# Kernel tuning notes

Measured on AMD Instinct MI355X. Metric: run time of the kernel, lower is better.

## Reference

```python
import jax, jax.numpy as jnp
import numpy as np

RANK = 16
ALPHA = 32
SCALING = ALPHA / RANK  # alpha / rank


def setup_inputs() -> dict:
    key = jax.random.key(0)
    k_x, k_w, k_b, k_a, k_bb = jax.random.split(key, 5)
    B, S, D_IN, D_OUT = 4, 2048, 4096, 4096
    x = jax.random.normal(k_x, (B, S, D_IN), dtype=jnp.float32)
    W = jax.random.normal(k_w, (D_OUT, D_IN), dtype=jnp.float32) * (1.0 / np.sqrt(D_IN))
    b = jax.random.normal(k_b, (D_OUT,), dtype=jnp.float32) * 0.02
    # LoRA init: A ~ N(0, 2/rank); B is zeros in the module, but we use small
    # random values so the adapter path is numerically exercised.
    lora_A = jax.random.normal(k_a, (RANK, D_IN), dtype=jnp.float32) * np.sqrt(2.0 / RANK)
    lora_B = jax.random.normal(k_bb, (D_OUT, RANK), dtype=jnp.float32) * 0.02
    return {"x": x, "W": W, "b": b, "lora_A": lora_A, "lora_B": lora_B}


def reference(x, W, b, lora_A, lora_B):
    # Base linear: x @ W^T + b
    base = jnp.einsum("bsd,od->bso", x, W) + b
    # LoRA path, fused as two rank-r matmuls (never materializing B@A):
    # (x @ A^T) @ B^T * scaling  ==  F.linear(x, B@A) * scaling
    xa = jnp.einsum("bsd,rd->bsr", x, lora_A)      # [B,S,r]
    lora = jnp.einsum("bsr,or->bso", xa, lora_B)    # [B,S,D_out]
    return base + lora * SCALING
```

## Files before the change

kernel.cpp:

```cpp
#include <hip/hip_runtime.h>
#include <hip/hip_bf16.h>

#define K_DIM 4096
#define N_DIM 4096
#define R_DIM 16
#define SCALING_F 2.0f

#define BM 256
#define BN 256
#define BK 64

typedef __attribute__((ext_vector_type(8))) short bf16x8;
typedef __attribute__((ext_vector_type(16))) float f32x16;

__device__ __forceinline__ ushort f2bf(float f) {
  union { float f; unsigned u; } v; v.f = f;
  unsigned u = v.u;
  u += 0x7FFF + ((u >> 16) & 1);
  return (ushort)(u >> 16);
}

__global__ __launch_bounds__(256) void prepass_kernel(
    const float* __restrict__ x, ushort* __restrict__ xb,
    const float* __restrict__ W, const float* __restrict__ A,
    const float* __restrict__ Bl, ushort* __restrict__ wb, long n4) {
  if (blockIdx.x < N_DIM) {
    int o = blockIdx.x;
    float breg[R_DIM];
#pragma unroll
    for (int r = 0; r < R_DIM; ++r) breg[r] = Bl[o * R_DIM + r] * SCALING_F;
    for (int d0 = threadIdx.x * 4; d0 < K_DIM; d0 += blockDim.x * 4) {
      float4 w = *(const float4*)(W + (size_t)o * K_DIM + d0);
      float a0 = w.x, a1 = w.y, a2 = w.z, a3 = w.w;
#pragma unroll
      for (int r = 0; r < R_DIM; ++r) {
        float4 a = *(const float4*)(A + (size_t)r * K_DIM + d0);
        a0 += breg[r] * a.x; a1 += breg[r] * a.y;
        a2 += breg[r] * a.z; a3 += breg[r] * a.w;
      }
      ushort4 ob;
      ob.x = f2bf(a0); ob.y = f2bf(a1); ob.z = f2bf(a2); ob.w = f2bf(a3);
      *(ushort4*)(wb + (size_t)o * K_DIM + d0) = ob;
    }
  } else {
    long i = (long)(blockIdx.x - N_DIM) * blockDim.x + threadIdx.x;
    long stride = 2048L * blockDim.x;
    for (; i < n4; i += stride) {
      long idx = i * 4;
      float4 v = *(const float4*)(x + idx);
      ushort4 o;
      o.x = f2bf(v.x); o.y = f2bf(v.y); o.z = f2bf(v.z); o.w = f2bf(v.w);
      *(ushort4*)(xb + idx) = o;
    }
  }
}


#define RS 8192L

#define GLOAD(SRC, LOFF)                                                    \
  __builtin_amdgcn_global_load_lds(                                         \
      (const __attribute__((address_space(1))) void*)(SRC),                 \
      (__attribute__((address_space(3))) void*)(smem + (LOFF)), 16, 0, 0)

#define LDSA(BUF) ((BUF) * 32768)
#define LDSB(BUF) (65536 + (BUF) * 32768)

#define ST_A_EVEN(T, BUF) do {                                              \
    GLOAD(aS + (size_t)(T) * 128,            LDSA(BUF) + ldsDst);           \
    GLOAD(aS + (size_t)(T) * 128 + 128 * RS, LDSA(BUF) + 16384 + ldsDst); } while (0)
#define ST_A_ODD(T, BUF) do {                                               \
    GLOAD(aS + (size_t)(T) * 128 + 64 * RS,  LDSA(BUF) + 8192 + ldsDst);    \
    GLOAD(aS + (size_t)(T) * 128 + 192 * RS, LDSA(BUF) + 24576 + ldsDst); } while (0)
#define ST_B_H0(T, BUF) do {                                                \
    GLOAD(bS + (size_t)(T) * 128,            LDSB(BUF) + ldsDst);           \
    GLOAD(bS + (size_t)(T) * 128 + 64 * RS,  LDSB(BUF) + 8192 + ldsDst); } while (0)
#define ST_B_H1(T, BUF) do {                                                \
    GLOAD(bS + (size_t)(T) * 128 + 128 * RS, LDSB(BUF) + 16384 + ldsDst);   \
    GLOAD(bS + (size_t)(T) * 128 + 192 * RS, LDSB(BUF) + 24576 + ldsDst); } while (0)

#define LDAx(MI, KS, BUF) (*(const bf16x8*)(smem + LDSA(BUF) + aRd + (MI) * 4096 + cs##KS))
#define LDBx(NI, KS, BUF) (*(const bf16x8*)(smem + LDSB(BUF) + bRd + (NI) * 4096 + cs##KS))

#define RDB_ALL(BUF) do {                                                   \
    bfr[0][0] = LDBx(0, 0, BUF); bfr[0][1] = LDBx(0, 1, BUF);               \
    bfr[0][2] = LDBx(0, 2, BUF); bfr[0][3] = LDBx(0, 3, BUF);               \
    bfr[1][0] = LDBx(1, 0, BUF); bfr[1][1] = LDBx(1, 1, BUF);               \
    bfr[1][2] = LDBx(1, 2, BUF); bfr[1][3] = LDBx(1, 3, BUF); } while (0)

#define RDA(MB, K0, K1, BUF) do {                                           \
    afr[0][0] = LDAx(MB, K0, BUF);       afr[0][1] = LDAx(MB, K1, BUF);     \
    afr[1][0] = LDAx((MB) + 1, K0, BUF); afr[1][1] = LDAx((MB) + 1, K1, BUF); } while (0)

#define MFMA8(MB, KH) do {                                                  \
    _Pragma("unroll") for (int mm = 0; mm < 2; ++mm)                        \
      _Pragma("unroll") for (int nn = 0; nn < 2; ++nn)                      \
        _Pragma("unroll") for (int kk = 0; kk < 2; ++kk)                    \
          acc[(MB) + mm][nn] = __builtin_amdgcn_mfma_f32_32x32x16_bf16(     \
              afr[mm][kk], bfr[nn][2 * (KH) + kk], acc[(MB) + mm][nn], 0, 0, 0); } while (0)

#define PH_MFMA(MB, KH) do {                                                \
    __builtin_amdgcn_s_barrier();                                           \
    asm volatile("s_waitcnt lgkmcnt(0)" ::: "memory");                      \
    __builtin_amdgcn_s_setprio(1);                                          \
    MFMA8(MB, KH);                                                          \
    __builtin_amdgcn_s_setprio(0); } while (0)

__global__ __launch_bounds__(512, 2) void gemm_lora_kernel(
    const ushort* __restrict__ Ab, const ushort* __restrict__ Bb,
    const float* __restrict__ bias, float* __restrict__ C) {
  __shared__ char smem[131072];

  const int tid = threadIdx.x;
  const int wave = tid >> 6, lane = tid & 63;
  const int wm = wave >> 2, wn = wave & 3;
  const int r31 = lane & 31, hi = lane >> 5;

  const int bid = blockIdx.x;
  const int bm = ((bid & 7) << 2) + ((bid >> 3) & 3);
  const int bn = bid >> 5;

  const int trow = tid >> 3;
  const int tswz = ((tid & 7) << 4) ^ ((trow & 7) << 4);
  const char* aS = (const char*)Ab + (size_t)(bm * BM + trow) * RS + tswz;
  const char* bS = (const char*)Bb + (size_t)(bn * BN + trow) * RS + tswz;
  const int ldsDst = tid << 4;

  const int hi16 = hi << 4;
  const int swz  = (lane & 7) << 4;
  const int cs0 = (0  + hi16) ^ swz;
  const int cs1 = (32 + hi16) ^ swz;
  const int cs2 = (64 + hi16) ^ swz;
  const int cs3 = (96 + hi16) ^ swz;
  const int aRd = (wm * 128 + r31) * 128;
  const int bRd = (wn * 64 + r31) * 128;

  f32x16 acc[4][2];
#pragma unroll
  for (int m = 0; m < 4; ++m)
#pragma unroll
    for (int n = 0; n < 2; ++n)
#pragma unroll
      for (int v = 0; v < 16; ++v) acc[m][n][v] = 0.f;
  bf16x8 afr[2][2], bfr[2][4];

  ST_B_H0(0, 0); ST_B_H1(0, 0); ST_A_EVEN(0, 0); ST_A_ODD(0, 0);
  ST_B_H0(1, 1); ST_B_H1(1, 1); ST_A_EVEN(1, 1);
  asm volatile("s_waitcnt vmcnt(6)" ::: "memory");
  __builtin_amdgcn_s_barrier();

  const int NIT = K_DIM / (2 * BK);
#pragma unroll 1
  for (int i = 0; i < NIT; ++i) {
    const int t1 = 2 * i + 1, t2 = 2 * i + 2, t3 = 2 * i + 3;
    const bool last = (i == NIT - 1);

    RDB_ALL(0);
    RDA(0, 0, 1, 0);
    ST_A_ODD(t1, 1);
    asm volatile("s_waitcnt lgkmcnt(8)" ::: "memory");
    PH_MFMA(0, 0);
    __builtin_amdgcn_s_barrier();

    RDA(0, 2, 3, 0);
    if (!last) ST_B_H0(t2, 0);
    PH_MFMA(0, 1);
    __builtin_amdgcn_s_barrier();

    RDA(2, 0, 1, 0);
    if (!last) ST_B_H1(t2, 0);
    PH_MFMA(2, 0);
    __builtin_amdgcn_s_barrier();

    RDA(2, 2, 3, 0);
    if (!last) ST_A_EVEN(t2, 0);
    PH_MFMA(2, 1);
    if (last) asm volatile("s_waitcnt vmcnt(0)" ::: "memory");
    else      asm volatile("s_waitcnt vmcnt(6)" ::: "memory");
    __builtin_amdgcn_s_barrier();

    RDB_ALL(1);
    RDA(0, 0, 1, 1);
    if (!last) ST_A_ODD(t2, 0);
    asm volatile("s_waitcnt lgkmcnt(8)" ::: "memory");
    PH_MFMA(0, 0);
    __builtin_amdgcn_s_barrier();

    RDA(0, 2, 3, 1);
    if (!last) ST_B_H0(t3, 1);
    PH_MFMA(0, 1);
    __builtin_amdgcn_s_barrier();

    RDA(2, 0, 1, 1);
    if (!last) ST_B_H1(t3, 1);
    PH_MFMA(2, 0);
    __builtin_amdgcn_s_barrier();

    RDA(2, 2, 3, 1);
    if (!last) ST_A_EVEN(t3, 1);
    PH_MFMA(2, 1);
    if (!last) {
      asm volatile("s_waitcnt vmcnt(6)" ::: "memory");
      __builtin_amdgcn_s_barrier();
    }
  }

  const int ccol0 = bn * BN + wn * 64 + r31;
  const float bv0 = bias[ccol0];
  const float bv1 = bias[ccol0 + 32];
  const int crow0 = bm * BM + wm * 128 + hi * 4;
#pragma unroll
  for (int mi = 0; mi < 4; ++mi)
#pragma unroll
    for (int v = 0; v < 16; ++v) {
      int row = crow0 + mi * 32 + (v & 3) + 8 * (v >> 2);
      C[(size_t)row * N_DIM + ccol0]      = acc[mi][0][v] + bv0;
      C[(size_t)row * N_DIM + ccol0 + 32] = acc[mi][1][v] + bv1;
    }
}

extern "C" void kernel_launch(void* const* d_in, const int* in_sizes, int n_in,
                              void* d_out, int out_size, void* d_ws, size_t ws_size,
                              hipStream_t stream) {
  const float* x  = (const float*)d_in[0];
  const float* W  = (const float*)d_in[1];
  const float* b  = (const float*)d_in[2];
  const float* lA = (const float*)d_in[3];
  const float* lB = (const float*)d_in[4];
  float* out = (float*)d_out;

  const int M = in_sizes[0] / K_DIM;

  ushort* xb = (ushort*)d_ws;
  ushort* wb = xb + (size_t)M * K_DIM;

  long n4 = (long)M * K_DIM / 4;
  prepass_kernel<<<N_DIM + 2048, 256, 0, stream>>>(x, xb, W, lA, lB, wb, n4);
  gemm_lora_kernel<<<(M / BM) * (N_DIM / BN), 512, 0, stream>>>(xb, wb, b, out);
}
```

Measured before the change: 340.9 us.

## Prefetch LDS fragments one phase ahead and move swizzle into prepass layout

Moves the XOR swizzle from the LDS load addressing into the global layout written by the bf16 prepass, so each 16-byte global_load_lds copies contiguously. Fragment reads now issue as two 8-byte LDS loads with a new swizzle pattern. A and B register fragments for the next MFMA phase are loaded right after the current phase's MFMAs, which overlaps LDS latency with compute. The vmcnt waits are retuned to match the reordered stores. The risks are more LDS instructions from the split 8-byte reads, possible bank conflicts, and the removed memory clobber on the lgkmcnt wait, which could let the compiler reorder LDS reads past it.

```diff
diff --git a/kernel.cpp b/kernel.cpp
--- a/kernel.cpp
+++ b/kernel.cpp
@@ -10,6 +10,7 @@
 #define BN 256
 #define BK 64
 
+typedef __attribute__((ext_vector_type(4))) short bf16x4;
 typedef __attribute__((ext_vector_type(8))) short bf16x8;
 typedef __attribute__((ext_vector_type(16))) float f32x16;
 
@@ -40,7 +41,8 @@
       }
       ushort4 ob;
       ob.x = f2bf(a0); ob.y = f2bf(a1); ob.z = f2bf(a2); ob.w = f2bf(a3);
-      *(ushort4*)(wb + (size_t)o * K_DIM + d0) = ob;
+      int cs = (d0 >> 2) ^ (o & 15);
+      *(ushort4*)(wb + (size_t)o * K_DIM + (cs << 2)) = ob;
     }
   } else {
     long i = (long)(blockIdx.x - N_DIM) * blockDim.x + threadIdx.x;
@@ -50,7 +52,9 @@
       float4 v = *(const float4*)(x + idx);
       ushort4 o;
       o.x = f2bf(v.x); o.y = f2bf(v.y); o.z = f2bf(v.z); o.w = f2bf(v.w);
-      *(ushort4*)(xb + idx) = o;
+      int row15 = (int)(idx >> 12) & 15;
+      int cs = (((int)idx & 4095) >> 2) ^ row15;
+      *(ushort4*)(xb + (idx & ~4095L) + ((long)cs << 2)) = o;
     }
   }
 }
@@ -79,18 +83,22 @@
     GLOAD(bS + (size_t)(T) * 128 + 128 * RS, LDSB(BUF) + 16384 + ldsDst);   \
     GLOAD(bS + (size_t)(T) * 128 + 192 * RS, LDSB(BUF) + 24576 + ldsDst); } while (0)
 
-#define LDAx(MI, KS, BUF) (*(const bf16x8*)(smem + LDSA(BUF) + aRd + (MI) * 4096 + cs##KS))
-#define LDBx(NI, KS, BUF) (*(const bf16x8*)(smem + LDSB(BUF) + bRd + (NI) * 4096 + cs##KS))
-
-#define RDB_ALL(BUF) do {                                                   \
-    bfr[0][0] = LDBx(0, 0, BUF); bfr[0][1] = LDBx(0, 1, BUF);               \
-    bfr[0][2] = LDBx(0, 2, BUF); bfr[0][3] = LDBx(0, 3, BUF);               \
-    bfr[1][0] = LDBx(1, 0, BUF); bfr[1][1] = LDBx(1, 1, BUF);               \
-    bfr[1][2] = LDBx(1, 2, BUF); bfr[1][3] = LDBx(1, 3, BUF); } while (0)
-
-#define RDA(MB, K0, K1, BUF) do {                                           \
-    afr[0][0] = LDAx(MB, K0, BUF);       afr[0][1] = LDAx(MB, K1, BUF);     \
-    afr[1][0] = LDAx((MB) + 1, K0, BUF); afr[1][1] = LDAx((MB) + 1, K1, BUF); } while (0)
+#define FR(BASE, OFF, KS)                                                   \
+  __builtin_shufflevector(                                                  \
+      *(const bf16x4*)(smem + (BASE) + (OFF) + cl[KS]),                     \
+      *(const bf16x4*)(smem + (BASE) + (OFF) + ch[KS]),                     \
+      0, 1, 2, 3, 4, 5, 6, 7)
+
+#define PF_A(MB, KH, BUF) do {                                              \
+    afr[0][0] = FR(aRow, (MB) * 4096 + (BUF) * 32768, 2 * (KH));            \
+    afr[0][1] = FR(aRow, (MB) * 4096 + (BUF) * 32768, 2 * (KH) + 1);        \
+    afr[1][0] = FR(aRow, ((MB) + 1) * 4096 + (BUF) * 32768, 2 * (KH));      \
+    afr[1][1] = FR(aRow, ((MB) + 1) * 4096 + (BUF) * 32768, 2 * (KH) + 1); } while (0)
+
+#define PF_B_ALL(BUF) do {                                                  \
+    _Pragma("unroll") for (int nt = 0; nt < 2; ++nt)                        \
+      _Pragma("unroll") for (int ks = 0; ks < 4; ++ks)                      \
+        bfr[nt][ks] = FR(bRow, nt * 4096 + (BUF) * 32768, ks); } while (0)
 
 #define MFMA8(MB, KH) do {                                                  \
     _Pragma("unroll") for (int mm = 0; mm < 2; ++mm)                        \
@@ -99,9 +107,9 @@
           acc[(MB) + mm][nn] = __builtin_amdgcn_mfma_f32_32x32x16_bf16(     \
               afr[mm][kk], bfr[nn][2 * (KH) + kk], acc[(MB) + mm][nn], 0, 0, 0); } while (0)
 
-#define PH_MFMA(MB, KH) do {                                                \
+#define PH_CORE(MB, KH) do {                                                \
     __builtin_amdgcn_s_barrier();                                           \
-    asm volatile("s_waitcnt lgkmcnt(0)" ::: "memory");                      \
+    asm volatile("s_waitcnt lgkmcnt(0)");                                   \
     __builtin_amdgcn_s_setprio(1);                                          \
     MFMA8(MB, KH);                                                          \
     __builtin_amdgcn_s_setprio(0); } while (0)
@@ -121,19 +129,22 @@
   const int bn = bid >> 5;
 
   const int trow = tid >> 3;
-  const int tswz = ((tid & 7) << 4) ^ ((trow & 7) << 4);
-  const char* aS = (const char*)Ab + (size_t)(bm * BM + trow) * RS + tswz;
-  const char* bS = (const char*)Bb + (size_t)(bn * BN + trow) * RS + tswz;
+  const char* aS = (const char*)Ab + (size_t)(bm * BM + trow) * RS + ((tid & 7) << 4);
+  const char* bS = (const char*)Bb + (size_t)(bn * BN + trow) * RS + ((tid & 7) << 4);
   const int ldsDst = tid << 4;
 
-  const int hi16 = hi << 4;
-  const int swz  = (lane & 7) << 4;
-  const int cs0 = (0  + hi16) ^ swz;
-  const int cs1 = (32 + hi16) ^ swz;
-  const int cs2 = (64 + hi16) ^ swz;
-  const int cs3 = (96 + hi16) ^ swz;
-  const int aRd = (wm * 128 + r31) * 128;
-  const int bRd = (wn * 64 + r31) * 128;
+  const int sxh = (r31 & 14) << 3;
+  const int sxb = (r31 & 1) << 3;
+  const int cl[4] = {(((0 * 2 + hi) << 4) ^ sxh) | sxb,
+                     (((1 * 2 + hi) << 4) ^ sxh) | sxb,
+                     (((2 * 2 + hi) << 4) ^ sxh) | sxb,
+                     (((3 * 2 + hi) << 4) ^ sxh) | sxb};
+  const int ch[4] = {(((0 * 2 + hi) << 4) ^ sxh) | (8 ^ sxb),
+                     (((1 * 2 + hi) << 4) ^ sxh) | (8 ^ sxb),
+                     (((2 * 2 + hi) << 4) ^ sxh) | (8 ^ sxb),
+                     (((3 * 2 + hi) << 4) ^ sxh) | (8 ^ sxb)};
+  const int aRow = (wm * 128 + r31) * 128;
+  const int bRow = 65536 + (wn * 64 + r31) * 128;
 
   f32x16 acc[4][2];
 #pragma unroll
@@ -148,6 +159,8 @@
   ST_B_H0(1, 1); ST_B_H1(1, 1); ST_A_EVEN(1, 1);
   asm volatile("s_waitcnt vmcnt(6)" ::: "memory");
   __builtin_amdgcn_s_barrier();
+  PF_B_ALL(0);
+  PF_A(0, 0, 0);
 
   const int NIT = K_DIM / (2 * BK);
 #pragma unroll 1
@@ -155,52 +168,50 @@
     const int t1 = 2 * i + 1, t2 = 2 * i + 2, t3 = 2 * i + 3;
     const bool last = (i == NIT - 1);
 
-    RDB_ALL(0);
-    RDA(0, 0, 1, 0);
     ST_A_ODD(t1, 1);
-    asm volatile("s_waitcnt lgkmcnt(8)" ::: "memory");
-    PH_MFMA(0, 0);
-    __builtin_amdgcn_s_barrier();
-
-    RDA(0, 2, 3, 0);
+    PH_CORE(0, 0);
+    PF_A(0, 1, 0);
+    __builtin_amdgcn_s_barrier();
+
     if (!last) ST_B_H0(t2, 0);
-    PH_MFMA(0, 1);
-    __builtin_amdgcn_s_barrier();
-
-    RDA(2, 0, 1, 0);
+    PH_CORE(0, 1);
+    PF_A(2, 0, 0);
+    __builtin_amdgcn_s_barrier();
+
     if (!last) ST_B_H1(t2, 0);
-    PH_MFMA(2, 0);
-    __builtin_amdgcn_s_barrier();
-
-    RDA(2, 2, 3, 0);
+    PH_CORE(2, 0);
+    PF_A(2, 1, 0);
+    if (last) asm volatile("s_waitcnt vmcnt(0)" ::: "memory");
+    else      asm volatile("s_waitcnt vmcnt(4)" ::: "memory");
+    __builtin_amdgcn_s_barrier();
+
     if (!last) ST_A_EVEN(t2, 0);
-    PH_MFMA(2, 1);
-    if (last) asm volatile("s_waitcnt vmcnt(0)" ::: "memory");
-    else      asm volatile("s_waitcnt vmcnt(6)" ::: "memory");
-    __builtin_amdgcn_s_barrier();
-
-    RDB_ALL(1);
-    RDA(0, 0, 1, 1);
+    PH_CORE(2, 1);
+    PF_B_ALL(1);
+    PF_A(0, 0, 1);
+    __builtin_amdgcn_s_barrier();
+
     if (!last) ST_A_ODD(t2, 0);
-    asm volatile("s_waitcnt lgkmcnt(8)" ::: "memory");
-    PH_MFMA(0, 0);
-    __builtin_amdgcn_s_barrier();
-
-    RDA(0, 2, 3, 1);
+    PH_CORE(0, 0);
+    PF_A(0, 1, 1);
+    __builtin_amdgcn_s_barrier();
+
     if (!last) ST_B_H0(t3, 1);
-    PH_MFMA(0, 1);
-    __builtin_amdgcn_s_barrier();
-
-    RDA(2, 0, 1, 1);
+    PH_CORE(0, 1);
+    PF_A(2, 0, 1);
+    __builtin_amdgcn_s_barrier();
+
     if (!last) ST_B_H1(t3, 1);
-    PH_MFMA(2, 0);
-    __builtin_amdgcn_s_barrier();
-
-    RDA(2, 2, 3, 1);
+    PH_CORE(2, 0);
+    PF_A(2, 1, 1);
+    if (!last) asm volatile("s_waitcnt vmcnt(4)" ::: "memory");
+    __builtin_amdgcn_s_barrier();
+
     if (!last) ST_A_EVEN(t3, 1);
-    PH_MFMA(2, 1);
+    PH_CORE(2, 1);
     if (!last) {
-      asm volatile("s_waitcnt vmcnt(6)" ::: "memory");
+      PF_B_ALL(0);
+      PF_A(0, 0, 0);
       __builtin_amdgcn_s_barrier();
     }
   }
```

Measured after the change: 352.2 us. +3.3%, slower.
